# Kernel optimization log

Hardware: AMD Instinct MI355X
Metric: run time of the kernel (lower is better)

The kernel has to match this reference:

```python
import jax, jax.numpy as jnp
import numpy as np

# FCHL19 hyperparameters (from init_kwargs defaults)
NSPEC = 4
RCUT = 6.0
NRS2 = 24
NRS3 = 20
ETA2 = 0.32
ETA3 = 2.7
TWO_BODY_DECAY = 1.8
THREE_BODY_WEIGHT = float(np.sqrt(2.7 / np.pi) * 13.4)  # sqrt(eta3/pi)*13.4, as in __init__
THREE_BODY_DECAY = 0.57
PI = float(np.pi)
NPAIRS = NSPEC * (NSPEC + 1) // 2  # 10 unordered element pairs
RS2 = jnp.linspace(0.0, RCUT, NRS2 + 1)[1:]
RS3 = jnp.linspace(0.0, RCUT, NRS3 + 1)[1:]


def setup_inputs() -> dict:
    key = jax.random.key(0)
    k1, k2, k3 = jax.random.split(key, 3)
    B, A = 64, 48
    X = jax.random.uniform(k1, (B, A, 3), jnp.float32, 0.0, 12.0)  # coords in 12 A box
    Z = jax.random.randint(k2, (B, A), 0, NSPEC, dtype=jnp.int32)  # species indices into [1,6,7,8]
    atom_counts = jax.random.randint(k3, (B,), 24, A + 1, dtype=jnp.int32)
    atomIDs = (jnp.arange(B * A, dtype=jnp.int32) % A)
    molIDs = (jnp.arange(B * A, dtype=jnp.int32) // A)
    return {"X": X, "Z": Z, "atomIDs": atomIDs, "molIDs": molIDs, "atom_counts": atom_counts}


def _fchl_rep(X, Z, atom_counts):
    B, A, _ = X.shape
    idx = jnp.arange(A)
    valid = idx[None, :] < atom_counts[:, None]                       # [B,A]
    diff = X[:, :, None, :] - X[:, None, :, :]                        # [B,A,A,3] (X_i - X_j)
    r2 = jnp.sum(diff * diff, axis=-1)
    eye = jnp.eye(A, dtype=bool)
    pmask = valid[:, :, None] & valid[:, None, :] & ~eye              # [B,A,A]
    r = jnp.sqrt(jnp.where(pmask, r2, 1.0))
    within = pmask & (r < RCUT)
    rs = jnp.where(within, r, 1.0)                                    # safe distances
    fc = jnp.where(within, 0.5 * (jnp.cos(PI * rs / RCUT) + 1.0), 0.0)

    # ---- two-body: log-normal radial basis with power-law scaling ----
    s2 = jnp.log1p(ETA2 / (rs * rs))                                  # sigma^2
    mu = jnp.log(rs) - 0.5 * s2
    pref = fc / (rs ** TWO_BODY_DECAY) / (jnp.sqrt(s2) * np.sqrt(2.0 * PI))
    radial2 = (pref[..., None] / RS2) * jnp.exp(
        -(jnp.log(RS2) - mu[..., None]) ** 2 / (2.0 * s2[..., None]))  # [B,A,A,nRs2]
    eoh = jax.nn.one_hot(Z, NSPEC, dtype=X.dtype) * valid[..., None]  # [B,A,S]
    rep2 = jnp.einsum('bijk,bjs->bisk', radial2, eoh).reshape(B, A, NSPEC * NRS2)

    # ---- three-body: ATM-weighted radial x (cos,sin) angular, pairs k>j ----
    rij = rs[:, :, :, None]   # [B,A(i),A(j),1]
    rik = rs[:, :, None, :]   # [B,A(i),1,A(k)]
    rjk = rs[:, None, :, :]   # [B,1,A(j),A(k)]
    cos_i = jnp.einsum('bijx,bikx->bijk', diff, diff) / (rij * rik)
    cos_i = jnp.clip(cos_i, -1.0, 1.0)
    cos_j = (rij * rij + rjk * rjk - rik * rik) / (2.0 * rij * rjk)
    cos_k = (rik * rik + rjk * rjk - rij * rij) / (2.0 * rik * rjk)
    mask3 = (within[:, :, :, None] & within[:, :, None, :]
             & (idx[None, :] > idx[:, None])[None, None, :, :])        # k > j
    ksi3 = THREE_BODY_WEIGHT * (1.0 + 3.0 * cos_i * cos_j * cos_k) \
        / (rij * rik * rjk) ** THREE_BODY_DECAY
    w = jnp.where(mask3, ksi3 * fc[:, :, :, None] * fc[:, :, None, :], 0.0)
    wc = w * cos_i
    ws = w * jnp.sqrt(jnp.clip(1.0 - cos_i * cos_i, 0.0, 1.0))
    d = 0.5 * (rij + rik)                                             # [B,A,A,A]

    # unordered element-pair bin for (Z_j, Z_k)
    ej = Z[:, :, None]
    ek = Z[:, None, :]
    pmin = jnp.minimum(ej, ek)
    pmax = jnp.maximum(ej, ek)
    pidx = pmin * (2 * NSPEC - pmin - 1) // 2 + pmax                  # [B,A,A]
    poh = jax.nn.one_hot(pidx, NPAIRS, dtype=X.dtype)                 # [B,A,A,P]

    def step(carry, Rl):
        rad = jnp.exp(-ETA3 * (d - Rl) ** 2)
        rc = jnp.einsum('bijk,bjkp->bip', wc * rad, poh)
        rsn = jnp.einsum('bijk,bjkp->bip', ws * rad, poh)
        return carry, jnp.stack([rc, rsn], axis=-1)                   # [B,A,P,2]

    _, rep3 = jax.lax.scan(step, 0, RS3)                              # [nRs3,B,A,P,2]
    rep3 = jnp.transpose(rep3, (1, 2, 3, 0, 4)).reshape(B, A, NPAIRS * NRS3 * 2)
    return jnp.concatenate([rep2, rep3], axis=-1)                     # [B,A,496]


def reference(X, Z, atomIDs, molIDs, atom_counts):
    # atomIDs/molIDs are CUDA work-distribution lists; math-irrelevant here.
    return _fchl_rep(X, Z, atom_counts)
```

## Files before the change

kernel.cpp:

```cpp
#include <hip/hip_runtime.h>
#include <math.h>

#define B_MOL 64
#define A_MAX 48
#define NSPEC 4
#define NRS2 24
#define NRS3 20
#define NPAIRS 10
#define REP2 (NSPEC * NRS2)
#define REP3 (NPAIRS * NRS3 * 2)
#define REPTOT (REP2 + REP3)
#define TRIP_CAP (A_MAX * (A_MAX - 1) / 2 + 1)

#define RCUT_F 6.0f
#define ETA2_F 0.32f
#define ETA3_F 2.7f
#define PI_F 3.14159265358979323846f
#define W3_F 12.4225780586f
#define SQRT_2PI_F 2.5066282746310002f

__global__ __launch_bounds__(256) void fchl_kernel(
    const float* __restrict__ X, const int* __restrict__ Z,
    const int* __restrict__ atom_counts, float* __restrict__ out)
{
    const int bi = blockIdx.x;
    const int b = bi / A_MAX;
    const int i = bi % A_MAX;
    const int tid = threadIdx.x;

    __shared__ float sx[A_MAX], sy[A_MAX], sz[A_MAX];
    __shared__ int   sZa[A_MAX];
    __shared__ float nb_dx[A_MAX], nb_dy[A_MAX], nb_dz[A_MAX], nb_r[A_MAX];
    __shared__ float nb_fc[A_MAX], nb_mu[A_MAX], nb_i2s2[A_MAX], nb_pref[A_MAX];
    __shared__ int   nb_z[A_MAX];
    __shared__ int   nb_m;
    __shared__ int   bcnt[NPAIRS], bstart[NPAIRS], bcur[NPAIRS];
    __shared__ float trip_wc[TRIP_CAP], trip_ws[TRIP_CAP], trip_d[TRIP_CAP];

    const int cnt = atom_counts[b];

    if (tid < A_MAX) {
        sx[tid]  = X[(b * A_MAX + tid) * 3 + 0];
        sy[tid]  = X[(b * A_MAX + tid) * 3 + 1];
        sz[tid]  = X[(b * A_MAX + tid) * 3 + 2];
        sZa[tid] = Z[b * A_MAX + tid];
    }
    if (tid < NPAIRS) bcnt[tid] = 0;
    __syncthreads();

    const float xi = sx[i], yi = sy[i], zi = sz[i];
    const bool ivalid = (i < cnt);

    if (tid < 64) {
        const int j = tid;
        bool flag = false;
        float dx = 0.f, dy = 0.f, dz = 0.f, r = 1.f;
        if (j < A_MAX) {
            dx = xi - sx[j]; dy = yi - sy[j]; dz = zi - sz[j];
            r = sqrtf(dx * dx + dy * dy + dz * dz);
            flag = ivalid && (j < cnt) && (j != i) && (r < RCUT_F);
        }
        const unsigned long long mask = __ballot(flag ? 1 : 0);
        if (flag) {
            const int pos = __popcll(mask & ((1ull << tid) - 1ull));
            nb_dx[pos] = dx; nb_dy[pos] = dy; nb_dz[pos] = dz;
            nb_r[pos]  = r;  nb_z[pos]  = sZa[j];
            const float fc = 0.5f * (__cosf(PI_F * r * (1.0f / RCUT_F)) + 1.0f);
            const float lr = __logf(r);
            const float s2 = log1pf(ETA2_F / (r * r));
            nb_fc[pos]   = fc;
            nb_mu[pos]   = lr - 0.5f * s2;
            nb_i2s2[pos] = 1.0f / (2.0f * s2);
            nb_pref[pos] = fc * __expf(-1.8f * lr) / (sqrtf(s2) * SQRT_2PI_F);
        }
        if (tid == 0) nb_m = (int)__popcll(mask);
    }
    __syncthreads();
    const int m = nb_m;
    const int ntrip = m * (m - 1) / 2;

    float* orow = out + (size_t)bi * REPTOT;

    if (tid < REP2) {
        const int s = tid / NRS2;
        const int n = tid % NRS2;
        const float Rn = 0.25f * (float)(n + 1);
        const float logRn = __logf(Rn);
        float acc = 0.0f;
        for (int a = 0; a < m; ++a) {
            if (nb_z[a] == s) {
                const float dmu = logRn - nb_mu[a];
                acc += nb_pref[a] * __expf(-dmu * dmu * nb_i2s2[a]);
            }
        }
        orow[tid] = acc * (1.0f / Rn);
    }

    for (int t = tid; t < ntrip; t += 256) {
        int rem = t, a = 0, rl = m - 1;
        while (rem >= rl) { rem -= rl; --rl; ++a; }
        const int c = a + 1 + rem;
        const int zj = nb_z[a], zk = nb_z[c];
        const int pmn = min(zj, zk), pmx = max(zj, zk);
        const int p = (pmn * (2 * NSPEC - pmn - 1)) / 2 + pmx;
        atomicAdd(&bcnt[p], 1);
    }
    __syncthreads();
    if (tid == 0) {
        int s = 0;
        for (int p = 0; p < NPAIRS; ++p) { bstart[p] = s; bcur[p] = s; s += bcnt[p]; }
    }
    __syncthreads();

    for (int t = tid; t < ntrip; t += 256) {
        int rem = t, a = 0, rl = m - 1;
        while (rem >= rl) { rem -= rl; --rl; ++a; }
        const int c = a + 1 + rem;

        const float rij = nb_r[a], rik = nb_r[c];
        const float djx = nb_dx[a], djy = nb_dy[a], djz = nb_dz[a];
        const float dkx = nb_dx[c], dky = nb_dy[c], dkz = nb_dz[c];

        float cosi = (djx * dkx + djy * dky + djz * dkz) / (rij * rik);
        cosi = fminf(1.0f, fmaxf(-1.0f, cosi));

        const float ex = dkx - djx, ey = dky - djy, ez = dkz - djz;
        const float rjk = sqrtf(ex * ex + ey * ey + ez * ez);
        const float rjke = (rjk < RCUT_F) ? rjk : 1.0f;

        const float cosj = (rij * rij + rjke * rjke - rik * rik) / (2.0f * rij * rjke);
        const float cosk = (rik * rik + rjke * rjke - rij * rij) / (2.0f * rik * rjke);

        const float ksi = W3_F * (1.0f + 3.0f * cosi * cosj * cosk)
                        * __expf(-0.57f * __logf(rij * rik * rjke));
        const float w  = ksi * nb_fc[a] * nb_fc[c];
        const float wc = w * cosi;
        const float s1 = fmaxf(1.0f - cosi * cosi, 0.0f);
        const float ws = w * sqrtf(s1);
        const float d  = 0.5f * (rij + rik);

        const int zj = nb_z[a], zk = nb_z[c];
        const int pmn = min(zj, zk), pmx = max(zj, zk);
        const int p = (pmn * (2 * NSPEC - pmn - 1)) / 2 + pmx;

        const int slot = atomicAdd(&bcur[p], 1);
        trip_wc[slot] = wc; trip_ws[slot] = ws; trip_d[slot] = d;
    }
    __syncthreads();

    if (tid < NPAIRS * NRS3) {
        const int p = tid / NRS3;
        const int l = tid % NRS3;
        const float Rl = 0.3f * (float)(l + 1);
        const int s0 = bstart[p];
        const int s1 = s0 + bcnt[p];
        float ac = 0.0f, as_ = 0.0f;
        for (int s = s0; s < s1; ++s) {
            const float dd = trip_d[s] - Rl;
            const float rad = __expf(-ETA3_F * dd * dd);
            ac  += trip_wc[s] * rad;
            as_ += trip_ws[s] * rad;
        }
        orow[REP2 + p * (NRS3 * 2) + l * 2 + 0] = ac;
        orow[REP2 + p * (NRS3 * 2) + l * 2 + 1] = as_;
    }
}

extern "C" void kernel_launch(void* const* d_in, const int* in_sizes, int n_in,
                              void* d_out, int out_size, void* d_ws, size_t ws_size,
                              hipStream_t stream) {
    const float* X           = (const float*)d_in[0];
    const int*   Z           = (const int*)d_in[1];
    const int*   atom_counts = (const int*)d_in[4];
    float* out = (float*)d_out;

    fchl_kernel<<<B_MOL * A_MAX, 256, 0, stream>>>(X, Z, atom_counts, out);
}
```

Before: 74.41 us.

## Closed-form triplet decode, precomputed bin slots, packed float4 triplets, overlapped two-body

The serial triangle-index loop is replaced with a closed-form sqrt decode. Each triplet's bin and in-bin rank are recorded during the counting pass, so the second atomic pass is gone. Triplet data is packed into one float4 array, and divides and square roots become hardware rcp/sqrt intrinsics. The two-body basis is moved onto the 56 threads that sit idle during the three-body accumulation phase. The trade-offs are slightly lower numerical accuracy from the approximate intrinsics and reliance on float rounding in the decode, which is guarded by correction loops.

```diff
diff --git a/kernel.cpp b/kernel.cpp
--- a/kernel.cpp
+++ b/kernel.cpp
@@ -10,7 +10,7 @@
 #define REP2 (NSPEC * NRS2)
 #define REP3 (NPAIRS * NRS3 * 2)
 #define REPTOT (REP2 + REP3)
-#define TRIP_CAP (A_MAX * (A_MAX - 1) / 2 + 1)
+#define TRIP_CAP 1084
 
 #define RCUT_F 6.0f
 #define ETA2_F 0.32f
@@ -18,6 +18,18 @@
 #define PI_F 3.14159265358979323846f
 #define W3_F 12.4225780586f
 #define SQRT_2PI_F 2.5066282746310002f
+
+__device__ __forceinline__ void decode_tri(int t, int m, int& a_out, int& c_out) {
+    const float fm = (float)(2 * m - 1);
+    const float disc = fm * fm - 8.0f * (float)t;
+    const float sq = __builtin_amdgcn_sqrtf(disc);
+    int a = (int)((fm - sq) * 0.5f);
+    if (a < 0) a = 0;
+    while (a > 0 && (a * (2 * m - 1 - a)) / 2 > t) --a;
+    while (((a + 1) * (2 * m - 1 - (a + 1))) / 2 <= t) ++a;
+    a_out = a;
+    c_out = t - (a * (2 * m - 1 - a)) / 2 + a + 1;
+}
 
 __global__ __launch_bounds__(256) void fchl_kernel(
     const float* __restrict__ X, const int* __restrict__ Z,
@@ -30,12 +42,14 @@
 
     __shared__ float sx[A_MAX], sy[A_MAX], sz[A_MAX];
     __shared__ int   sZa[A_MAX];
-    __shared__ float nb_dx[A_MAX], nb_dy[A_MAX], nb_dz[A_MAX], nb_r[A_MAX];
+    __shared__ float nb_dx[A_MAX], nb_dy[A_MAX], nb_dz[A_MAX];
+    __shared__ float nb_r[A_MAX], nb_r2[A_MAX], nb_rinv[A_MAX];
     __shared__ float nb_fc[A_MAX], nb_mu[A_MAX], nb_i2s2[A_MAX], nb_pref[A_MAX];
     __shared__ int   nb_z[A_MAX];
     __shared__ int   nb_m;
-    __shared__ int   bcnt[NPAIRS], bstart[NPAIRS], bcur[NPAIRS];
-    __shared__ float trip_wc[TRIP_CAP], trip_ws[TRIP_CAP], trip_d[TRIP_CAP];
+    __shared__ int   bcnt[NPAIRS], bstart[NPAIRS];
+    __shared__ unsigned short pq[TRIP_CAP];
+    __shared__ float4 trip[TRIP_CAP];
 
     const int cnt = atom_counts[b];
 
@@ -57,21 +71,24 @@
         float dx = 0.f, dy = 0.f, dz = 0.f, r = 1.f;
         if (j < A_MAX) {
             dx = xi - sx[j]; dy = yi - sy[j]; dz = zi - sz[j];
-            r = sqrtf(dx * dx + dy * dy + dz * dz);
+            r = __builtin_amdgcn_sqrtf(dx * dx + dy * dy + dz * dz);
             flag = ivalid && (j < cnt) && (j != i) && (r < RCUT_F);
         }
         const unsigned long long mask = __ballot(flag ? 1 : 0);
         if (flag) {
             const int pos = __popcll(mask & ((1ull << tid) - 1ull));
             nb_dx[pos] = dx; nb_dy[pos] = dy; nb_dz[pos] = dz;
-            nb_r[pos]  = r;  nb_z[pos]  = sZa[j];
+            nb_r[pos]  = r;  nb_r2[pos] = r * r;
+            nb_rinv[pos] = __builtin_amdgcn_rcpf(r);
+            nb_z[pos]  = sZa[j];
             const float fc = 0.5f * (__cosf(PI_F * r * (1.0f / RCUT_F)) + 1.0f);
             const float lr = __logf(r);
             const float s2 = log1pf(ETA2_F / (r * r));
             nb_fc[pos]   = fc;
             nb_mu[pos]   = lr - 0.5f * s2;
-            nb_i2s2[pos] = 1.0f / (2.0f * s2);
-            nb_pref[pos] = fc * __expf(-1.8f * lr) / (sqrtf(s2) * SQRT_2PI_F);
+            nb_i2s2[pos] = 0.5f * __builtin_amdgcn_rcpf(s2);
+            nb_pref[pos] = fc * __expf(-1.8f * lr) *
+                           __builtin_amdgcn_rcpf(__builtin_amdgcn_sqrtf(s2) * SQRT_2PI_F);
         }
         if (tid == 0) nb_m = (int)__popcll(mask);
     }
@@ -81,70 +98,57 @@
 
     float* orow = out + (size_t)bi * REPTOT;
 
-    if (tid < REP2) {
-        const int s = tid / NRS2;
-        const int n = tid % NRS2;
-        const float Rn = 0.25f * (float)(n + 1);
-        const float logRn = __logf(Rn);
-        float acc = 0.0f;
-        for (int a = 0; a < m; ++a) {
-            if (nb_z[a] == s) {
-                const float dmu = logRn - nb_mu[a];
-                acc += nb_pref[a] * __expf(-dmu * dmu * nb_i2s2[a]);
-            }
-        }
-        orow[tid] = acc * (1.0f / Rn);
-    }
-
     for (int t = tid; t < ntrip; t += 256) {
-        int rem = t, a = 0, rl = m - 1;
-        while (rem >= rl) { rem -= rl; --rl; ++a; }
-        const int c = a + 1 + rem;
+        int a, c;
+        decode_tri(t, m, a, c);
         const int zj = nb_z[a], zk = nb_z[c];
         const int pmn = min(zj, zk), pmx = max(zj, zk);
         const int p = (pmn * (2 * NSPEC - pmn - 1)) / 2 + pmx;
-        atomicAdd(&bcnt[p], 1);
+        const int q = atomicAdd(&bcnt[p], 1);
+        pq[t] = (unsigned short)(p | (q << 4));
     }
     __syncthreads();
     if (tid == 0) {
         int s = 0;
-        for (int p = 0; p < NPAIRS; ++p) { bstart[p] = s; bcur[p] = s; s += bcnt[p]; }
+        for (int p = 0; p < NPAIRS; ++p) { bstart[p] = s; s += bcnt[p]; }
     }
     __syncthreads();
 
     for (int t = tid; t < ntrip; t += 256) {
-        int rem = t, a = 0, rl = m - 1;
-        while (rem >= rl) { rem -= rl; --rl; ++a; }
-        const int c = a + 1 + rem;
+        int a, c;
+        decode_tri(t, m, a, c);
 
         const float rij = nb_r[a], rik = nb_r[c];
+        const float r2ij = nb_r2[a], r2ik = nb_r2[c];
+        const float rinv_a = nb_rinv[a], rinv_c = nb_rinv[c];
         const float djx = nb_dx[a], djy = nb_dy[a], djz = nb_dz[a];
         const float dkx = nb_dx[c], dky = nb_dy[c], dkz = nb_dz[c];
 
-        float cosi = (djx * dkx + djy * dky + djz * dkz) / (rij * rik);
+        float cosi = (djx * dkx + djy * dky + djz * dkz) * rinv_a * rinv_c;
         cosi = fminf(1.0f, fmaxf(-1.0f, cosi));
 
         const float ex = dkx - djx, ey = dky - djy, ez = dkz - djz;
-        const float rjk = sqrtf(ex * ex + ey * ey + ez * ez);
-        const float rjke = (rjk < RCUT_F) ? rjk : 1.0f;
+        const float rjk2 = ex * ex + ey * ey + ez * ez;
+        const float rjk = __builtin_amdgcn_sqrtf(rjk2);
+        const bool w_jk = (rjk < RCUT_F);
+        const float rjke  = w_jk ? rjk : 1.0f;
+        const float rjke2 = w_jk ? rjk2 : 1.0f;
+        const float rinv_jk = w_jk ? __builtin_amdgcn_rcpf(rjk) : 1.0f;
 
-        const float cosj = (rij * rij + rjke * rjke - rik * rik) / (2.0f * rij * rjke);
-        const float cosk = (rik * rik + rjke * rjke - rij * rij) / (2.0f * rik * rjke);
+        const float cosj = (r2ij + rjke2 - r2ik) * 0.5f * rinv_a * rinv_jk;
+        const float cosk = (r2ik + rjke2 - r2ij) * 0.5f * rinv_c * rinv_jk;
 
         const float ksi = W3_F * (1.0f + 3.0f * cosi * cosj * cosk)
                         * __expf(-0.57f * __logf(rij * rik * rjke));
         const float w  = ksi * nb_fc[a] * nb_fc[c];
         const float wc = w * cosi;
         const float s1 = fmaxf(1.0f - cosi * cosi, 0.0f);
-        const float ws = w * sqrtf(s1);
+        const float ws = w * __builtin_amdgcn_sqrtf(s1);
         const float d  = 0.5f * (rij + rik);
 
-        const int zj = nb_z[a], zk = nb_z[c];
-        const int pmn = min(zj, zk), pmx = max(zj, zk);
-        const int p = (pmn * (2 * NSPEC - pmn - 1)) / 2 + pmx;
-
-        const int slot = atomicAdd(&bcur[p], 1);
-        trip_wc[slot] = wc; trip_ws[slot] = ws; trip_d[slot] = d;
+        const unsigned short e = pq[t];
+        const int slot = bstart[e & 15] + (int)(e >> 4);
+        trip[slot] = make_float4(wc, ws, d, 0.0f);
     }
     __syncthreads();
 
@@ -156,13 +160,29 @@
         const int s1 = s0 + bcnt[p];
         float ac = 0.0f, as_ = 0.0f;
         for (int s = s0; s < s1; ++s) {
-            const float dd = trip_d[s] - Rl;
+            const float4 v = trip[s];
+            const float dd = v.z - Rl;
             const float rad = __expf(-ETA3_F * dd * dd);
-            ac  += trip_wc[s] * rad;
-            as_ += trip_ws[s] * rad;
+            ac  += v.x * rad;
+            as_ += v.y * rad;
         }
         orow[REP2 + p * (NRS3 * 2) + l * 2 + 0] = ac;
         orow[REP2 + p * (NRS3 * 2) + l * 2 + 1] = as_;
+    } else {
+        for (int t2 = tid - 200; t2 < REP2; t2 += 56) {
+            const int s = t2 / NRS2;
+            const int n = t2 % NRS2;
+            const float Rn = 0.25f * (float)(n + 1);
+            const float logRn = __logf(Rn);
+            float acc = 0.0f;
+            for (int a = 0; a < m; ++a) {
+                if (nb_z[a] == s) {
+                    const float dmu = logRn - nb_mu[a];
+                    acc += nb_pref[a] * __expf(-dmu * dmu * nb_i2s2[a]);
+                }
+            }
+            orow[t2] = acc * __builtin_amdgcn_rcpf(Rn);
+        }
     }
 }
 
```

New measurement: 76.04 us. 2.2% more time.
